# Performance work log

Measured on AMD Instinct MI355X. Metric: run time of the kernel, lower is better.

The kernel has to match this reference:

```python
import jax, jax.numpy as jnp
import numpy as np
from jax import lax

INPUT_DIM = 12
T = 2048
H = 512
L = 6
EPS = 1e-5


def setup_inputs() -> dict:
    key = jax.random.key(0)
    ks = jax.random.split(key, 12)
    s = 1.0 / np.sqrt(H)
    inp = {
        "x": jax.random.normal(ks[0], (32, INPUT_DIM), dtype=jnp.float32),
        "in_proj_w": jax.random.normal(ks[1], (H, INPUT_DIM), dtype=jnp.float32) * (1.0 / np.sqrt(INPUT_DIM)),
        "in_proj_b": jnp.zeros((H,), dtype=jnp.float32),
        "W_ih": jax.random.uniform(ks[2], (L, 4 * H, H), dtype=jnp.float32, minval=-s, maxval=s),
        "W_hh": jax.random.uniform(ks[3], (L, 4 * H, H), dtype=jnp.float32, minval=-s, maxval=s),
        "b_ih": jax.random.uniform(ks[4], (L, 4 * H), dtype=jnp.float32, minval=-s, maxval=s),
        "b_hh": jax.random.uniform(ks[5], (L, 4 * H), dtype=jnp.float32, minval=-s, maxval=s),
        "ln_scale": jnp.ones((L, H), dtype=jnp.float32),
        "ln_bias": jnp.zeros((L, H), dtype=jnp.float32),
        "out_w": jax.random.normal(ks[6], (1, H), dtype=jnp.float32) * s,
        "out_b": jnp.zeros((1,), dtype=jnp.float32),
    }
    return inp


def _lstm_layer(h_in, Wih, Whh, bih, bhh):
    # h_in: (B, T, H); PyTorch gate order: i, f, g, o
    B = h_in.shape[0]
    xg = jnp.einsum("bth,gh->btg", h_in, Wih) + bih  # (B, T, 4H) input gates precomputed
    xg_t = jnp.swapaxes(xg, 0, 1)  # (T, B, 4H)
    h0 = jnp.zeros((B, H), dtype=h_in.dtype)
    c0 = jnp.zeros((B, H), dtype=h_in.dtype)

    def step(carry, xt):
        h, c = carry
        gates = xt + h @ Whh.T + bhh
        i, f, g, o = jnp.split(gates, 4, axis=-1)
        i = jax.nn.sigmoid(i)
        f = jax.nn.sigmoid(f)
        g = jnp.tanh(g)
        o = jax.nn.sigmoid(o)
        c = f * c + i * g
        h = o * jnp.tanh(c)
        return (h, c), h

    _, hs = lax.scan(step, (h0, c0), xg_t)  # hs: (T, B, H)
    return jnp.swapaxes(hs, 0, 1)


def _layernorm(x, scale, bias):
    mu = jnp.mean(x, axis=-1, keepdims=True)
    var = jnp.mean(jnp.square(x - mu), axis=-1, keepdims=True)
    return (x - mu) * lax.rsqrt(var + EPS) * scale + bias


def reference(x, in_proj_w, in_proj_b, W_ih, W_hh, b_ih, b_hh, ln_scale, ln_bias, out_w, out_b):
    x_proj = x @ in_proj_w.T + in_proj_b  # (B, H)
    h = jnp.broadcast_to(x_proj[:, None, :], (x.shape[0], T, H))  # repeat along time
    for l in range(L):
        out = _lstm_layer(h, W_ih[l], W_hh[l], b_ih[l], b_hh[l])
        h = _layernorm(out + h, ln_scale[l], ln_bias[l])  # dropout = identity (eval)
    y = jnp.einsum("bth,oh->bto", h, out_w) + out_b  # (B, T, 1)
    return y[..., 0]  # (B, T)
```

## Files before the change

kernel.cpp:

```cpp
#include <hip/hip_runtime.h>

typedef __attribute__((ext_vector_type(4))) int   i32x4;
typedef __attribute__((ext_vector_type(8))) short s16x8;
typedef __attribute__((ext_vector_type(4))) float f32x4;

__device__ __forceinline__ unsigned short f2bf(float f) {
  unsigned u = __float_as_uint(f);
  unsigned r = u + 0x7FFFu + ((u >> 16) & 1u);
  return (unsigned short)(r >> 16);
}
__device__ __forceinline__ unsigned pack2bf(float lo, float hi) {
  return (unsigned)f2bf(lo) | ((unsigned)f2bf(hi) << 16);
}
__device__ __forceinline__ float bflo(unsigned u){ return __uint_as_float(u << 16); }
__device__ __forceinline__ float bfhi(unsigned u){ return __uint_as_float(u & 0xFFFF0000u); }

__device__ __forceinline__ float sigm(float x){ return 1.0f / (1.0f + __expf(-x)); }
__device__ __forceinline__ float tanh_(float x){
  float ax = fabsf(x);
  float e  = __expf(-2.0f * ax);
  float t  = (1.0f - e) / (1.0f + e);
  return copysignf(t, x);
}

__device__ __forceinline__ unsigned long long aload(const unsigned long long* p) {
  return __hip_atomic_load(p, __ATOMIC_RELAXED, __HIP_MEMORY_SCOPE_AGENT);
}
__device__ __forceinline__ void astore32(unsigned* p, unsigned v) {
  __hip_atomic_store(p, v, __ATOMIC_RELAXED, __HIP_MEMORY_SCOPE_AGENT);
}

__device__ __forceinline__ void waitflags(const unsigned* F, int base, unsigned need, int lane) {
  const unsigned* p = F + base + (lane & 31);
  unsigned v = __hip_atomic_load(p, __ATOMIC_RELAXED, __HIP_MEMORY_SCOPE_AGENT);
  while (!__all((int)(v >= need))) {
    __builtin_amdgcn_s_sleep(1);
    v = __hip_atomic_load(p, __ATOMIC_RELAXED, __HIP_MEMORY_SCOPE_AGENT);
  }
}

__global__ __launch_bounds__(256) void k_inproj(const float* __restrict__ x,
                                                const float* __restrict__ w,
                                                const float* __restrict__ bb,
                                                float* __restrict__ XP) {
  int idx = blockIdx.x * 256 + threadIdx.x;
  int b = idx >> 9, j = idx & 511;
  float acc = bb[j];
#pragma unroll
  for (int k = 0; k < 12; ++k) acc += x[b * 12 + k] * w[j * 12 + k];
  XP[idx] = acc;
}

__global__ __launch_bounds__(256) void k_xg0(const float* __restrict__ XP,
                                             const float* __restrict__ Wih,
                                             const float* __restrict__ bih,
                                             float* __restrict__ XG0) {
  int idx = blockIdx.x * 256 + threadIdx.x;
  int b = idx & 31;
  int r = idx >> 5;
  const float* wr = Wih + (size_t)r * 512;
  const float* xr = XP + b * 512;
  float acc = bih[r];
  for (int k = 0; k < 512; k += 4) {
    const f32x4 w4 = *(const f32x4*)(wr + k);
    const f32x4 x4 = *(const f32x4*)(xr + k);
    acc += w4[0]*x4[0] + w4[1]*x4[1] + w4[2]*x4[2] + w4[3]*x4[3];
  }
  XG0[b * 2048 + r] = acc;
}

__global__ __launch_bounds__(256, 1) void k_pipe(
    const float* __restrict__ Wih, const float* __restrict__ Whh,
    const float* __restrict__ bih, const float* __restrict__ bhh,
    const float* __restrict__ lnS, const float* __restrict__ lnB,
    const float* __restrict__ XG0, const float* __restrict__ XP,
    unsigned long long* __restrict__ Hst,
    unsigned long long* __restrict__ Roll,
    unsigned* __restrict__ RB,
    unsigned* __restrict__ Flg,
    unsigned* __restrict__ Prog)
{
  __shared__ char smem[74752];
  const int tid   = threadIdx.x;
  const int wgid  = blockIdx.x;
  const int layer = wgid >> 5;
  const int w     = wgid & 31;

  char* xarea = smem;
  char* harea = smem + 32768;
  float* gacc = (float*)(smem + 65536);
  const int lane = tid & 63;
  const int wv   = tid >> 6;
  const int j0   = w << 4;

  unsigned long long* HstL = Hst + layer * 8192;

  s16x8 bfih[16], bfhh[16];
  {
    const int rcol = lane & 15;
    const int kg   = lane >> 4;
    const size_t rowbase = ((size_t)layer * 2048 + (size_t)(wv * 512 + j0 + rcol)) * 512;
    const float* ihr = Wih + rowbase;
    const float* hhr = Whh + rowbase;
#pragma unroll
    for (int kk = 0; kk < 16; ++kk) {
      const int k0 = kg * 8 + kk * 32;
      s16x8 v2;
#pragma unroll
      for (int j = 0; j < 8; ++j) v2[j] = (short)f2bf(hhr[k0 + j]);
      bfhh[kk] = v2;
      if (layer > 0) {
        s16x8 v1;
#pragma unroll
        for (int j = 0; j < 8; ++j) v1[j] = (short)f2bf(ihr[k0 + j]);
        bfih[kk] = v1;
      }
    }
  }

  const int ub = tid >> 3;
  const int jp = tid & 7;
  const int kpglob = (j0 >> 1) + jp;

  float bs[4][2];
#pragma unroll
  for (int g = 0; g < 4; ++g)
#pragma unroll
    for (int c = 0; c < 2; ++c) {
      const size_t r = (size_t)layer * 2048 + g * 512 + j0 + 2 * jp + c;
      float vv = bhh[r];
      if (layer > 0) vv += bih[r];
      bs[g][c] = vv;
    }

  const float* lnSl = lnS + (layer - 1) * 512;
  const float* lnBl = lnB + (layer - 1) * 512;

  if (layer == 0) {
    float* xg0s = (float*)smem;
    float* xps  = (float*)(smem + 8192);
    for (int i = tid; i < 2048; i += 256) {
      int g = i >> 9, b = (i >> 4) & 31, jl = i & 15;
      xg0s[i] = XG0[b * 2048 + g * 512 + j0 + jl];
    }
    for (int i = tid; i < 512; i += 256) {
      int b = i >> 4, jl = i & 15;
      xps[i] = XP[b * 512 + j0 + jl];
    }
  }

  astore32((unsigned*)HstL + (ub << 8) + kpglob, 0u);
  __syncthreads();
  if (tid == 0)
    __hip_atomic_store(Flg + layer * 32 + w, 1u, __ATOMIC_RELEASE, __HIP_MEMORY_SCOPE_AGENT);

  float xinc0 = 0.f, xinc1 = 0.f;
  if (layer == 0) {
    const float* xps = (const float*)(smem + 8192);
    xinc0 = xps[ub * 16 + 2 * jp];
    xinc1 = xps[ub * 16 + 2 * jp + 1];
  }

  const int rr  = tid >> 3;
  const int kk8 = tid & 7;

  if (layer > 0) {
    waitflags(Flg, (layer - 1) * 32, 2u, lane);
    const unsigned long long* RollC = Roll + (layer - 1) * 16384;
    unsigned long long xr[16];
#pragma unroll
    for (int j = 0; j < 16; ++j) xr[j] = aload(RollC + rr * 128 + kk8 + 8 * j);
    float s = 0.f, ss = 0.f;
#pragma unroll
    for (int j = 0; j < 16; ++j) {
      const unsigned lo = (unsigned)xr[j], hi = (unsigned)(xr[j] >> 32);
      const float v0 = bflo(lo), v1 = bfhi(lo), v2 = bflo(hi), v3 = bfhi(hi);
      s  += v0 + v1 + v2 + v3;
      ss += v0 * v0 + v1 * v1 + v2 * v2 + v3 * v3;
    }
#pragma unroll
    for (int m = 1; m < 8; m <<= 1) { s += __shfl_xor(s, m, 64); ss += __shfl_xor(ss, m, 64); }
    const float mu = s * (1.f / 512.f);
    const float rs = rsqrtf(ss * (1.f / 512.f) - mu * mu + 1e-5f);
#pragma unroll
    for (int j = 0; j < 16; ++j) {
      const int jj = kk8 + 8 * j;
      const f32x4 sc4 = *(const f32x4*)(lnSl + 4 * jj);
      const f32x4 bi4 = *(const f32x4*)(lnBl + 4 * jj);
      const unsigned lo = (unsigned)xr[j], hi = (unsigned)(xr[j] >> 32);
      const float a0 = (bflo(lo) - mu) * rs * sc4[0] + bi4[0];
      const float a1 = (bfhi(lo) - mu) * rs * sc4[1] + bi4[1];
      const float a2 = (bflo(hi) - mu) * rs * sc4[2] + bi4[2];
      const float a3 = (bfhi(hi) - mu) * rs * sc4[3] + bi4[3];
      *(unsigned long long*)(xarea + ((rr * 1024 + jj * 8) ^ ((rr & 7) << 4))) =
          (unsigned long long)pack2bf(a0, a1) | ((unsigned long long)pack2bf(a2, a3) << 32);
    }
  }
  __syncthreads();

  const int rA  = lane & 15;
  const int kg2 = lane >> 4;
  const int swz = (rA & 7) << 4;
  const int ab0 = rA * 1024 + kg2 * 16;
  const int ab1 = ab0 + 16384;

  float creg0 = 0.f, creg1 = 0.f;
  unsigned myC = 0;
  unsigned prodC = 0;
  const int lane31 = lane & 31;

#pragma unroll 1
  for (int t = 0; t < 2048; ++t) {
    if (layer < 5 && t >= 5) {
      const unsigned need = (unsigned)(t - 4);
      while (!__all((int)(myC >= need))) {
        if (myC < need)
          myC = __hip_atomic_load(Prog + (layer + 1) * 32 + lane31,
                                  __ATOMIC_RELAXED, __HIP_MEMORY_SCOPE_AGENT);
        if (!__all((int)(myC >= need))) __builtin_amdgcn_s_sleep(1);
      }
    }

    waitflags(Flg, layer * 32, (unsigned)(t + 1), lane);

    const unsigned long long* hs = HstL + (size_t)(t & 1) * 4096;
    unsigned long long a[16];
#pragma unroll
    for (int it = 0; it < 16; ++it)
      a[it] = aload(hs + it * 256 + tid);

    unsigned long long xr[16];
    if (layer > 0 && t < 2047) {
      const unsigned need = (unsigned)(t + 3);
      while (!__all((int)(prodC >= need))) {
        if (prodC < need)
          prodC = __hip_atomic_load(Flg + (layer - 1) * 32 + lane31,
                                    __ATOMIC_RELAXED, __HIP_MEMORY_SCOPE_AGENT);
        if (!__all((int)(prodC >= need))) __builtin_amdgcn_s_sleep(1);
      }
      const unsigned long long* RollC = Roll + (size_t)((layer - 1) * 4 + ((t + 1) & 3)) * 4096;
#pragma unroll
      for (int j = 0; j < 16; ++j) xr[j] = aload(RollC + rr * 128 + kk8 + 8 * j);
    }

    float xin0, xin1;
    f32x4 ai0 = {0.f,0.f,0.f,0.f}, ai1 = {0.f,0.f,0.f,0.f};
    if (layer > 0) {
      const unsigned xu = *(const unsigned*)(xarea + (((ub * 1024) + kpglob * 4) ^ ((ub & 7) << 4)));
      xin0 = bflo(xu); xin1 = bfhi(xu);
#pragma unroll
      for (int kk = 0; kk < 16; ++kk) {
        const i32x4 x0 = *(const i32x4*)(xarea + ((ab0 + kk * 64) ^ swz));
        const i32x4 x1 = *(const i32x4*)(xarea + ((ab1 + kk * 64) ^ swz));
        ai0 = __builtin_amdgcn_mfma_f32_16x16x32_bf16(__builtin_bit_cast(s16x8, x0), bfih[kk], ai0, 0, 0, 0);
        ai1 = __builtin_amdgcn_mfma_f32_16x16x32_bf16(__builtin_bit_cast(s16x8, x1), bfih[kk], ai1, 0, 0, 0);
      }
    } else { xin0 = xinc0; xin1 = xinc1; }

#pragma unroll
    for (int it = 0; it < 16; ++it) {
      const int flat = it * 256 + tid;
      const int q = flat >> 7, kp2 = flat & 127;
      *(unsigned long long*)(harea + ((q * 1024 + kp2 * 8) ^ ((q & 7) << 4))) = a[it];
    }
    __syncthreads();

    f32x4 acc0, acc1;
    if (layer > 0) {
      f32x4 ah0 = {0.f,0.f,0.f,0.f}, ah1 = {0.f,0.f,0.f,0.f};
#pragma unroll
      for (int kk = 0; kk < 16; ++kk) {
        const i32x4 h0 = *(const i32x4*)(harea + ((ab0 + kk * 64) ^ swz));
        const i32x4 h1 = *(const i32x4*)(harea + ((ab1 + kk * 64) ^ swz));
        ah0 = __builtin_amdgcn_mfma_f32_16x16x32_bf16(__builtin_bit_cast(s16x8, h0), bfhh[kk], ah0, 0, 0, 0);
        ah1 = __builtin_amdgcn_mfma_f32_16x16x32_bf16(__builtin_bit_cast(s16x8, h1), bfhh[kk], ah1, 0, 0, 0);
      }
      acc0 = ai0 + ah0; acc1 = ai1 + ah1;
    } else {
      f32x4 a0a = {0.f,0.f,0.f,0.f}, a1a = {0.f,0.f,0.f,0.f};
      f32x4 a0b = {0.f,0.f,0.f,0.f}, a1b = {0.f,0.f,0.f,0.f};
#pragma unroll
      for (int kk = 0; kk < 8; ++kk) {
        const i32x4 h0a = *(const i32x4*)(harea + ((ab0 + kk * 64) ^ swz));
        const i32x4 h1a = *(const i32x4*)(harea + ((ab1 + kk * 64) ^ swz));
        const i32x4 h0b = *(const i32x4*)(harea + ((ab0 + (kk + 8) * 64) ^ swz));
        const i32x4 h1b = *(const i32x4*)(harea + ((ab1 + (kk + 8) * 64) ^ swz));
        a0a = __builtin_amdgcn_mfma_f32_16x16x32_bf16(__builtin_bit_cast(s16x8, h0a), bfhh[kk], a0a, 0, 0, 0);
        a1a = __builtin_amdgcn_mfma_f32_16x16x32_bf16(__builtin_bit_cast(s16x8, h1a), bfhh[kk], a1a, 0, 0, 0);
        a0b = __builtin_amdgcn_mfma_f32_16x16x32_bf16(__builtin_bit_cast(s16x8, h0b), bfhh[kk + 8], a0b, 0, 0, 0);
        a1b = __builtin_amdgcn_mfma_f32_16x16x32_bf16(__builtin_bit_cast(s16x8, h1b), bfhh[kk + 8], a1b, 0, 0, 0);
      }
      acc0 = a0a + a0b; acc1 = a1a + a1b;
    }
    {
      float* gp = gacc + (wv * 16 + rA) * 36 + kg2 * 4;
      *(f32x4*)gp        = acc0;
      *(f32x4*)(gp + 16) = acc1;
    }
    __syncthreads();

    float pre[4][2];
#pragma unroll
    for (int g = 0; g < 4; ++g)
#pragma unroll
      for (int c = 0; c < 2; ++c) {
        float vv = gacc[(g * 16 + 2 * jp + c) * 36 + ub] + bs[g][c];
        if (layer == 0) vv += ((const float*)smem)[(g * 32 + ub) * 16 + 2 * jp + c];
        pre[g][c] = vv;
      }

    float i0 = sigm(pre[0][0]), ff0 = sigm(pre[1][0]), g0 = tanh_(pre[2][0]), o0 = sigm(pre[3][0]);
    creg0 = ff0 * creg0 + i0 * g0;
    float h0 = o0 * tanh_(creg0);
    float i1 = sigm(pre[0][1]), ff1 = sigm(pre[1][1]), g1 = tanh_(pre[2][1]), o1 = sigm(pre[3][1]);
    creg1 = ff1 * creg1 + i1 * g1;
    float h1 = o1 * tanh_(creg1);
    const float out0 = h0 + xin0, out1 = h1 + xin1;

    if (layer < 5) {
      astore32((unsigned*)(Roll + (size_t)(layer * 4 + (t & 3)) * 4096) + (ub << 8) + kpglob,
               pack2bf(out0, out1));
    } else {
      RB[((size_t)ub * 2048 + t) * 256 + kpglob] = pack2bf(out0, out1);
    }
    astore32((unsigned*)(HstL + (size_t)((t + 1) & 1) * 4096) + (ub << 8) + kpglob,
             pack2bf(h0, h1));

    __syncthreads();
    if (tid == 0) {
      __hip_atomic_store(Flg + layer * 32 + w, (unsigned)(t + 2),
                         __ATOMIC_RELEASE, __HIP_MEMORY_SCOPE_AGENT);
      if (layer > 0 && t < 2047)
        astore32(Prog + layer * 32 + w, (unsigned)(t + 1));
    }

    if (layer > 0 && t < 2047) {
      float s = 0.f, ss = 0.f;
#pragma unroll
      for (int j = 0; j < 16; ++j) {
        const unsigned lo = (unsigned)xr[j], hi = (unsigned)(xr[j] >> 32);
        const float v0 = bflo(lo), v1 = bfhi(lo), v2 = bflo(hi), v3 = bfhi(hi);
        s  += v0 + v1 + v2 + v3;
        ss += v0 * v0 + v1 * v1 + v2 * v2 + v3 * v3;
      }
#pragma unroll
      for (int m = 1; m < 8; m <<= 1) { s += __shfl_xor(s, m, 64); ss += __shfl_xor(ss, m, 64); }
      const float mu = s * (1.f / 512.f);
      const float rs = rsqrtf(ss * (1.f / 512.f) - mu * mu + 1e-5f);
#pragma unroll
      for (int j = 0; j < 16; ++j) {
        const int jj = kk8 + 8 * j;
        const f32x4 sc4 = *(const f32x4*)(lnSl + 4 * jj);
        const f32x4 bi4 = *(const f32x4*)(lnBl + 4 * jj);
        const unsigned lo = (unsigned)xr[j], hi = (unsigned)(xr[j] >> 32);
        const float a0 = (bflo(lo) - mu) * rs * sc4[0] + bi4[0];
        const float a1 = (bfhi(lo) - mu) * rs * sc4[1] + bi4[1];
        const float a2 = (bflo(hi) - mu) * rs * sc4[2] + bi4[2];
        const float a3 = (bfhi(hi) - mu) * rs * sc4[3] + bi4[3];
        *(unsigned long long*)(xarea + ((rr * 1024 + jj * 8) ^ ((rr & 7) << 4))) =
            (unsigned long long)pack2bf(a0, a1) | ((unsigned long long)pack2bf(a2, a3) << 32);
      }
    }

    __syncthreads();
  }
}

__global__ __launch_bounds__(256) void k_lnout(const unsigned* __restrict__ Rin,
                                               const float* __restrict__ lnS,
                                               const float* __restrict__ lnB,
                                               const float* __restrict__ ow,
                                               const float* __restrict__ ob,
                                               float* __restrict__ y) {
  int row  = blockIdx.x * 4 + (threadIdx.x >> 6);
  int lane = threadIdx.x & 63;
  const i32x4 v = *(const i32x4*)(Rin + (size_t)row * 256 + lane * 4);
  float xv[8];
#pragma unroll
  for (int j = 0; j < 4; ++j) {
    unsigned u = (unsigned)v[j];
    xv[2*j]   = bflo(u);
    xv[2*j+1] = bfhi(u);
  }
  float s = 0.f, s2 = 0.f;
#pragma unroll
  for (int j = 0; j < 8; ++j) { s += xv[j]; s2 += xv[j] * xv[j]; }
#pragma unroll
  for (int m = 1; m < 64; m <<= 1) { s += __shfl_xor(s, m, 64); s2 += __shfl_xor(s2, m, 64); }
  float mu  = s * (1.f / 512.f);
  float var = s2 * (1.f / 512.f) - mu * mu;
  float rs  = rsqrtf(var + 1e-5f);
  const float* Sp = lnS + 5 * 512 + lane * 8;
  const float* Bp = lnB + 5 * 512 + lane * 8;
  const float* wp = ow + lane * 8;
  float acc = 0.f;
#pragma unroll
  for (int j = 0; j < 8; ++j)
    acc += ((xv[j] - mu) * rs * Sp[j] + Bp[j]) * wp[j];
#pragma unroll
  for (int m = 1; m < 64; m <<= 1) acc += __shfl_xor(acc, m, 64);
  if (lane == 0) y[row] = acc + ob[0];
}

extern "C" void kernel_launch(void* const* d_in, const int* in_sizes, int n_in,
                              void* d_out, int out_size, void* d_ws, size_t ws_size,
                              hipStream_t stream) {
  (void)in_sizes; (void)n_in; (void)out_size; (void)ws_size;
  const float* x   = (const float*)d_in[0];
  const float* ipw = (const float*)d_in[1];
  const float* ipb = (const float*)d_in[2];
  const float* Wih = (const float*)d_in[3];
  const float* Whh = (const float*)d_in[4];
  const float* bih = (const float*)d_in[5];
  const float* bhh = (const float*)d_in[6];
  const float* lnS = (const float*)d_in[7];
  const float* lnB = (const float*)d_in[8];
  const float* ow  = (const float*)d_in[9];
  const float* ob  = (const float*)d_in[10];
  float* y = (float*)d_out;

  char* ws = (char*)d_ws;
  unsigned* Flg             = (unsigned*)ws;
  unsigned* Prog            = (unsigned*)(ws + 1024);
  float* XP                 = (float*)(ws + 32768);
  float* XG0                = (float*)(ws + 98304);
  unsigned long long* Hst   = (unsigned long long*)(ws + 360448);
  unsigned long long* Roll  = (unsigned long long*)(ws + 753664);
  unsigned* RB              = (unsigned*)(ws + 2097152);

  hipMemsetAsync(ws, 0, 4096, stream);
  k_inproj<<<64, 256, 0, stream>>>(x, ipw, ipb, XP);
  k_xg0<<<256, 256, 0, stream>>>(XP, Wih, bih, XG0);
  k_pipe<<<192, 256, 0, stream>>>(Wih, Whh, bih, bhh, lnS, lnB, XG0, XP,
                                  Hst, Roll, RB, Flg, Prog);
  k_lnout<<<16384, 256, 0, stream>>>(RB, lnS, lnB, ow, ob, y);
}
```

Baseline: 16.50 ms.

## Halve per-layer workgroups to 16 with 512 threads each in LSTM pipeline

Changes the persistent pipelined LSTM kernel from 32 workgroups of 256 threads per layer to 16 workgroups of 512 threads, each owning 32 hidden units split across two wave halves. The aim is fewer cross-workgroup flag waits and less global h-state traffic per step, since each step's barrier now involves half as many producers. In exchange, each workgroup has more threads to synchronize per step and a larger LDS footprint. The layer-0 MFMA path loses its split-accumulator variant and now uses the same loop as the other layers.

Measured after the change: 25.41 ms. 54.0% more time.

```diff
diff --git a/kernel.cpp b/kernel.cpp
--- a/kernel.cpp
+++ b/kernel.cpp
@@ -31,7 +31,7 @@
 }
 
 __device__ __forceinline__ void waitflags(const unsigned* F, int base, unsigned need, int lane) {
-  const unsigned* p = F + base + (lane & 31);
+  const unsigned* p = F + base + (lane & 15);
   unsigned v = __hip_atomic_load(p, __ATOMIC_RELAXED, __HIP_MEMORY_SCOPE_AGENT);
   while (!__all((int)(v >= need))) {
     __builtin_amdgcn_s_sleep(1);
@@ -69,7 +69,7 @@
   XG0[b * 2048 + r] = acc;
 }
 
-__global__ __launch_bounds__(256, 1) void k_pipe(
+__global__ __launch_bounds__(512, 1) void k_pipe(
     const float* __restrict__ Wih, const float* __restrict__ Whh,
     const float* __restrict__ bih, const float* __restrict__ bhh,
     const float* __restrict__ lnS, const float* __restrict__ lnB,
@@ -80,18 +80,20 @@
     unsigned* __restrict__ Flg,
     unsigned* __restrict__ Prog)
 {
-  __shared__ char smem[74752];
+  __shared__ char smem[83968];
   const int tid   = threadIdx.x;
   const int wgid  = blockIdx.x;
-  const int layer = wgid >> 5;
-  const int w     = wgid & 31;
+  const int layer = wgid >> 4;
+  const int w     = wgid & 15;
 
   char* xarea = smem;
   char* harea = smem + 32768;
   float* gacc = (float*)(smem + 65536);
   const int lane = tid & 63;
   const int wv   = tid >> 6;
-  const int j0   = w << 4;
+  const int gt   = wv >> 1;
+  const int ch   = wv & 1;
+  const int j0   = w << 5;
 
   unsigned long long* HstL = Hst + layer * 8192;
 
@@ -99,7 +101,7 @@
   {
     const int rcol = lane & 15;
     const int kg   = lane >> 4;
-    const size_t rowbase = ((size_t)layer * 2048 + (size_t)(wv * 512 + j0 + rcol)) * 512;
+    const size_t rowbase = ((size_t)layer * 2048 + (size_t)(gt * 512 + j0 + ch * 16 + rcol)) * 512;
     const float* ihr = Wih + rowbase;
     const float* hhr = Whh + rowbase;
 #pragma unroll
@@ -118,8 +120,8 @@
     }
   }
 
-  const int ub = tid >> 3;
-  const int jp = tid & 7;
+  const int ub = tid >> 4;
+  const int jp = tid & 15;
   const int kpglob = (j0 >> 1) + jp;
 
   float bs[4][2];
@@ -138,13 +140,13 @@
 
   if (layer == 0) {
     float* xg0s = (float*)smem;
-    float* xps  = (float*)(smem + 8192);
-    for (int i = tid; i < 2048; i += 256) {
-      int g = i >> 9, b = (i >> 4) & 31, jl = i & 15;
+    float* xps  = (float*)(smem + 16384);
+    for (int i = tid; i < 4096; i += 512) {
+      int g = i >> 10, b = (i >> 5) & 31, jl = i & 31;
       xg0s[i] = XG0[b * 2048 + g * 512 + j0 + jl];
     }
-    for (int i = tid; i < 512; i += 256) {
-      int b = i >> 4, jl = i & 15;
+    for (int i = tid; i < 1024; i += 512) {
+      int b = i >> 5, jl = i & 31;
       xps[i] = XP[b * 512 + j0 + jl];
     }
   }
@@ -152,39 +154,39 @@
   astore32((unsigned*)HstL + (ub << 8) + kpglob, 0u);
   __syncthreads();
   if (tid == 0)
-    __hip_atomic_store(Flg + layer * 32 + w, 1u, __ATOMIC_RELEASE, __HIP_MEMORY_SCOPE_AGENT);
+    __hip_atomic_store(Flg + layer * 16 + w, 1u, __ATOMIC_RELEASE, __HIP_MEMORY_SCOPE_AGENT);
 
   float xinc0 = 0.f, xinc1 = 0.f;
   if (layer == 0) {
-    const float* xps = (const float*)(smem + 8192);
-    xinc0 = xps[ub * 16 + 2 * jp];
-    xinc1 = xps[ub * 16 + 2 * jp + 1];
-  }
-
-  const int rr  = tid >> 3;
-  const int kk8 = tid & 7;
+    const float* xps = (const float*)(smem + 16384);
+    xinc0 = xps[ub * 32 + 2 * jp];
+    xinc1 = xps[ub * 32 + 2 * jp + 1];
+  }
+
+  const int rr  = tid >> 4;
+  const int kk8 = tid & 15;
 
   if (layer > 0) {
-    waitflags(Flg, (layer - 1) * 32, 2u, lane);
+    waitflags(Flg, (layer - 1) * 16, 2u, lane);
     const unsigned long long* RollC = Roll + (layer - 1) * 16384;
-    unsigned long long xr[16];
-#pragma unroll
-    for (int j = 0; j < 16; ++j) xr[j] = aload(RollC + rr * 128 + kk8 + 8 * j);
+    unsigned long long xr[8];
+#pragma unroll
+    for (int j = 0; j < 8; ++j) xr[j] = aload(RollC + rr * 128 + kk8 + 16 * j);
     float s = 0.f, ss = 0.f;
 #pragma unroll
-    for (int j = 0; j < 16; ++j) {
+    for (int j = 0; j < 8; ++j) {
       const unsigned lo = (unsigned)xr[j], hi = (unsigned)(xr[j] >> 32);
       const float v0 = bflo(lo), v1 = bfhi(lo), v2 = bflo(hi), v3 = bfhi(hi);
       s  += v0 + v1 + v2 + v3;
       ss += v0 * v0 + v1 * v1 + v2 * v2 + v3 * v3;
     }
 #pragma unroll
-    for (int m = 1; m < 8; m <<= 1) { s += __shfl_xor(s, m, 64); ss += __shfl_xor(ss, m, 64); }
+    for (int m = 1; m < 16; m <<= 1) { s += __shfl_xor(s, m, 64); ss += __shfl_xor(ss, m, 64); }
     const float mu = s * (1.f / 512.f);
     const float rs = rsqrtf(ss * (1.f / 512.f) - mu * mu + 1e-5f);
 #pragma unroll
-    for (int j = 0; j < 16; ++j) {
-      const int jj = kk8 + 8 * j;
+    for (int j = 0; j < 8; ++j) {
+      const int jj = kk8 + 16 * j;
       const f32x4 sc4 = *(const f32x4*)(lnSl + 4 * jj);
       const f32x4 bi4 = *(const f32x4*)(lnBl + 4 * jj);
       const unsigned lo = (unsigned)xr[j], hi = (unsigned)(xr[j] >> 32);
@@ -207,7 +209,7 @@
   float creg0 = 0.f, creg1 = 0.f;
   unsigned myC = 0;
   unsigned prodC = 0;
-  const int lane31 = lane & 31;
+  const int lane15 = lane & 15;
 
 #pragma unroll 1
   for (int t = 0; t < 2048; ++t) {
@@ -215,32 +217,32 @@
       const unsigned need = (unsigned)(t - 4);
       while (!__all((int)(myC >= need))) {
         if (myC < need)
-          myC = __hip_atomic_load(Prog + (layer + 1) * 32 + lane31,
+          myC = __hip_atomic_load(Prog + (layer + 1) * 16 + lane15,
                                   __ATOMIC_RELAXED, __HIP_MEMORY_SCOPE_AGENT);
         if (!__all((int)(myC >= need))) __builtin_amdgcn_s_sleep(1);
       }
     }
 
-    waitflags(Flg, layer * 32, (unsigned)(t + 1), lane);
+    waitflags(Flg, layer * 16, (unsigned)(t + 1), lane);
 
     const unsigned long long* hs = HstL + (size_t)(t & 1) * 4096;
-    unsigned long long a[16];
-#pragma unroll
-    for (int it = 0; it < 16; ++it)
-      a[it] = aload(hs + it * 256 + tid);
-
-    unsigned long long xr[16];
+    unsigned long long a[8];
+#pragma unroll
+    for (int it = 0; it < 8; ++it)
+      a[it] = aload(hs + it * 512 + tid);
+
+    unsigned long long xr[8];
     if (layer > 0 && t < 2047) {
       const unsigned need = (unsigned)(t + 3);
       while (!__all((int)(prodC >= need))) {
         if (prodC < need)
-          prodC = __hip_atomic_load(Flg + (layer - 1) * 32 + lane31,
+          prodC = __hip_atomic_load(Flg + (layer - 1) * 16 + lane15,
                                     __ATOMIC_RELAXED, __HIP_MEMORY_SCOPE_AGENT);
         if (!__all((int)(prodC >= need))) __builtin_amdgcn_s_sleep(1);
       }
       const unsigned long long* RollC = Roll + (size_t)((layer - 1) * 4 + ((t + 1) & 3)) * 4096;
 #pragma unroll
-      for (int j = 0; j < 16; ++j) xr[j] = aload(RollC + rr * 128 + kk8 + 8 * j);
+      for (int j = 0; j < 8; ++j) xr[j] = aload(RollC + rr * 128 + kk8 + 16 * j);
     }
 
     float xin0, xin1;
@@ -258,42 +260,24 @@
     } else { xin0 = xinc0; xin1 = xinc1; }
 
 #pragma unroll
-    for (int it = 0; it < 16; ++it) {
-      const int flat = it * 256 + tid;
+    for (int it = 0; it < 8; ++it) {
+      const int flat = it * 512 + tid;
       const int q = flat >> 7, kp2 = flat & 127;
       *(unsigned long long*)(harea + ((q * 1024 + kp2 * 8) ^ ((q & 7) << 4))) = a[it];
     }
     __syncthreads();
 
-    f32x4 acc0, acc1;
-    if (layer > 0) {
-      f32x4 ah0 = {0.f,0.f,0.f,0.f}, ah1 = {0.f,0.f,0.f,0.f};
-#pragma unroll
-      for (int kk = 0; kk < 16; ++kk) {
-        const i32x4 h0 = *(const i32x4*)(harea + ((ab0 + kk * 64) ^ swz));
-        const i32x4 h1 = *(const i32x4*)(harea + ((ab1 + kk * 64) ^ swz));
-        ah0 = __builtin_amdgcn_mfma_f32_16x16x32_bf16(__builtin_bit_cast(s16x8, h0), bfhh[kk], ah0, 0, 0, 0);
-        ah1 = __builtin_amdgcn_mfma_f32_16x16x32_bf16(__builtin_bit_cast(s16x8, h1), bfhh[kk], ah1, 0, 0, 0);
-      }
-      acc0 = ai0 + ah0; acc1 = ai1 + ah1;
-    } else {
-      f32x4 a0a = {0.f,0.f,0.f,0.f}, a1a = {0.f,0.f,0.f,0.f};
-      f32x4 a0b = {0.f,0.f,0.f,0.f}, a1b = {0.f,0.f,0.f,0.f};
-#pragma unroll
-      for (int kk = 0; kk < 8; ++kk) {
-        const i32x4 h0a = *(const i32x4*)(harea + ((ab0 + kk * 64) ^ swz));
-        const i32x4 h1a = *(const i32x4*)(harea + ((ab1 + kk * 64) ^ swz));
-        const i32x4 h0b = *(const i32x4*)(harea + ((ab0 + (kk + 8) * 64) ^ swz));
-        const i32x4 h1b = *(const i32x4*)(harea + ((ab1 + (kk + 8) * 64) ^ swz));
-        a0a = __builtin_amdgcn_mfma_f32_16x16x32_bf16(__builtin_bit_cast(s16x8, h0a), bfhh[kk], a0a, 0, 0, 0);
-        a1a = __builtin_amdgcn_mfma_f32_16x16x32_bf16(__builtin_bit_cast(s16x8, h1a), bfhh[kk], a1a, 0, 0, 0);
-        a0b = __builtin_amdgcn_mfma_f32_16x16x32_bf16(__builtin_bit_cast(s16x8, h0b), bfhh[kk + 8], a0b, 0, 0, 0);
-        a1b = __builtin_amdgcn_mfma_f32_16x16x32_bf16(__builtin_bit_cast(s16x8, h1b), bfhh[kk + 8], a1b, 0, 0, 0);
-      }
-      acc0 = a0a + a0b; acc1 = a1a + a1b;
-    }
+    f32x4 ah0 = {0.f,0.f,0.f,0.f}, ah1 = {0.f,0.f,0.f,0.f};
+#pragma unroll
+    for (int kk = 0; kk < 16; ++kk) {
+      const i32x4 h0 = *(const i32x4*)(harea + ((ab0 + kk * 64) ^ swz));
+      const i32x4 h1 = *(const i32x4*)(harea + ((ab1 + kk * 64) ^ swz));
+      ah0 = __builtin_amdgcn_mfma_f32_16x16x32_bf16(__builtin_bit_cast(s16x8, h0), bfhh[kk], ah0, 0, 0, 0);
+      ah1 = __builtin_amdgcn_mfma_f32_16x16x32_bf16(__builtin_bit_cast(s16x8, h1), bfhh[kk], ah1, 0, 0, 0);
+    }
+    const f32x4 acc0 = ai0 + ah0, acc1 = ai1 + ah1;
     {
-      float* gp = gacc + (wv * 16 + rA) * 36 + kg2 * 4;
+      float* gp = gacc + (gt * 32 + ch * 16 + rA) * 36 + kg2 * 4;
       *(f32x4*)gp        = acc0;
       *(f32x4*)(gp + 16) = acc1;
     }
@@ -304,8 +288,8 @@
     for (int g = 0; g < 4; ++g)
 #pragma unroll
       for (int c = 0; c < 2; ++c) {
-        float vv = gacc[(g * 16 + 2 * jp + c) * 36 + ub] + bs[g][c];
-        if (layer == 0) vv += ((const float*)smem)[(g * 32 + ub) * 16 + 2 * jp + c];
+        float vv = gacc[(g * 32 + 2 * jp + c) * 36 + ub] + bs[g][c];
+        if (layer == 0) vv += ((const float*)smem)[g * 1024 + ub * 32 + 2 * jp + c];
         pre[g][c] = vv;
       }
 
@@ -328,28 +312,28 @@
 
     __syncthreads();
     if (tid == 0) {
-      __hip_atomic_store(Flg + layer * 32 + w, (unsigned)(t + 2),
+      __hip_atomic_store(Flg + layer * 16 + w, (unsigned)(t + 2),
                          __ATOMIC_RELEASE, __HIP_MEMORY_SCOPE_AGENT);
       if (layer > 0 && t < 2047)
-        astore32(Prog + layer * 32 + w, (unsigned)(t + 1));
+        astore32(Prog + layer * 16 + w, (unsigned)(t + 1));
     }
 
     if (layer > 0 && t < 2047) {
       float s = 0.f, ss = 0.f;
 #pragma unroll
-      for (int j = 0; j < 16; ++j) {
+      for (int j = 0; j < 8; ++j) {
         const unsigned lo = (unsigned)xr[j], hi = (unsigned)(xr[j] >> 32);
         const float v0 = bflo(lo), v1 = bfhi(lo), v2 = bflo(hi), v3 = bfhi(hi);
         s  += v0 + v1 + v2 + v3;
         ss += v0 * v0 + v1 * v1 + v2 * v2 + v3 * v3;
       }
 #pragma unroll
-      for (int m = 1; m < 8; m <<= 1) { s += __shfl_xor(s, m, 64); ss += __shfl_xor(ss, m, 64); }
+      for (int m = 1; m < 16; m <<= 1) { s += __shfl_xor(s, m, 64); ss += __shfl_xor(ss, m, 64); }
       const float mu = s * (1.f / 512.f);
       const float rs = rsqrtf(ss * (1.f / 512.f) - mu * mu + 1e-5f);
 #pragma unroll
-      for (int j = 0; j < 16; ++j) {
-        const int jj = kk8 + 8 * j;
+      for (int j = 0; j < 8; ++j) {
+        const int jj = kk8 + 16 * j;
         const f32x4 sc4 = *(const f32x4*)(lnSl + 4 * jj);
         const f32x4 bi4 = *(const f32x4*)(lnBl + 4 * jj);
         const unsigned lo = (unsigned)xr[j], hi = (unsigned)(xr[j] >> 32);
@@ -431,7 +415,7 @@
   hipMemsetAsync(ws, 0, 4096, stream);
   k_inproj<<<64, 256, 0, stream>>>(x, ipw, ipb, XP);
   k_xg0<<<256, 256, 0, stream>>>(XP, Wih, bih, XG0);
-  k_pipe<<<192, 256, 0, stream>>>(Wih, Whh, bih, bhh, lnS, lnB, XG0, XP,
-                                  Hst, Roll, RB, Flg, Prog);
+  k_pipe<<<96, 512, 0, stream>>>(Wih, Whh, bih, bhh, lnS, lnB, XG0, XP,
+                                 Hst, Roll, RB, Flg, Prog);
   k_lnout<<<16384, 256, 0, stream>>>(RB, lnS, lnB, ow, ob, y);
 }
```
